# Kernel tuning notes

Hardware: AMD Instinct MI355X
Metric: run time of the kernel (lower is better)

## Reference

```python
import jax, jax.numpy as jnp
import numpy as np

N = 131072  # nodes
E = 4096    # edges (unused by forward)
MID = 32    # multiplicity of irreps_mid = 32x0e + 32x1o
NF = 128    # multiplicity of node_feat_irreps = 128x0e + 128x1o
INV_SQRT3 = 0.5773502691896258          # |w3j(1,1,0)| = |w3j(0,1,1)| = 1/sqrt(3)
PW_QQ_S = (1.0 / 2048.0) ** 0.5         # path weight: alpha = dim(0e)/ (32*32 + 32*32)
PW_QQ_V = (3.0 / 2048.0) ** 0.5         # path weight: alpha = dim(1o)/ (32*32 + 32*32)
PW_DOWN = (1.0 / 8192.0) ** 0.5         # path weight: alpha = dim(0e)/ (32*128 + 32*128)


def setup_inputs() -> dict:
    key = jax.random.key(0)
    ks = jax.random.split(key, 20)
    inp = {
        "node_feats": jax.random.normal(ks[0], (N, NF + 3 * NF), jnp.float32),
        "charges_0": jax.random.normal(ks[1], (N, 4), jnp.float32),
        "charges_induced": jax.random.normal(ks[2], (N, 4), jnp.float32),
        "edge_feats": jax.random.normal(ks[3], (E, 8), jnp.float32),
        "edge_attrs": jax.random.normal(ks[4], (E, 9), jnp.float32),
        "field_feats": jax.random.normal(ks[5], (N, 4), jnp.float32),
        "edge_index": jax.random.randint(ks[6], (2, E), 0, N, dtype=jnp.int32),
        "batch": jnp.sort(jax.random.randint(ks[7], (N,), 0, 64, dtype=jnp.int32)),
        # o3.Linear(1x0e+1x1o -> 32x0e+32x1o) params (fan_in = 1 per path -> norm 1)
        "Wa_s": jax.random.normal(ks[8], (1, MID), jnp.float32),
        "Wa_v": jax.random.normal(ks[9], (1, MID), jnp.float32),
        "b_a": jnp.zeros((MID,), jnp.float32),
        "Wb_s": jax.random.normal(ks[10], (1, MID), jnp.float32),
        "Wb_v": jax.random.normal(ks[11], (1, MID), jnp.float32),
        "b_b": jnp.zeros((MID,), jnp.float32),
        # FullyConnectedTensorProduct(mid, mid -> mid) uvw weights, one per CG path
        "W_ss": jax.random.normal(ks[12], (MID, MID, MID), jnp.float32),  # 0e x 0e -> 0e
        "W_vv": jax.random.normal(ks[13], (MID, MID, MID), jnp.float32),  # 1o x 1o -> 0e
        "W_sv": jax.random.normal(ks[14], (MID, MID, MID), jnp.float32),  # 0e x 1o -> 1o
        "W_vs": jax.random.normal(ks[15], (MID, MID, MID), jnp.float32),  # 1o x 0e -> 1o
        # FullyConnectedTensorProduct(mid, node_feats -> 1x0e) uvw weights
        "Wd_s": jax.random.normal(ks[16], (MID, NF), jnp.float32),        # 0e x 0e -> 0e
        "Wd_v": jax.random.normal(ks[17], (MID, NF), jnp.float32),        # 1o x 1o -> 0e
    }
    return inp


def reference(node_feats, charges_0, charges_induced, edge_feats, edge_attrs,
              field_feats, edge_index, batch,
              Wa_s, Wa_v, b_a, Wb_s, Wb_v, b_b,
              W_ss, W_vv, W_sv, W_vs, Wd_s, Wd_v):
    # split irreps blocks
    s0, v0 = charges_0[:, :1], charges_0[:, 1:4]            # [N,1], [N,3]
    si, vi = charges_induced[:, :1], charges_induced[:, 1:4]
    nf_s = node_feats[:, :NF]                               # [N,128]
    nf_v = node_feats[:, NF:].reshape(-1, NF, 3)            # [N,128,3]

    # charges = linear_qa(charges_induced) + linear_qb(charges_0)  (bias only on 0e)
    s = si @ Wa_s + b_a + s0 @ Wb_s + b_b                   # [N,32]
    v = (jnp.einsum('nui,uw->nwi', vi[:, None, :], Wa_v)
         + jnp.einsum('nui,uw->nwi', v0[:, None, :], Wb_v))  # [N,32,3]

    # qq = FullyConnectedTensorProduct(charges, charges) -> 32x0e + 32x1o
    qs = PW_QQ_S * (jnp.einsum('nu,nv,uvw->nw', s, s, W_ss)
                    + INV_SQRT3 * jnp.einsum('nui,nvi,uvw->nw', v, v, W_vv))      # [N,32]
    qv = (PW_QQ_V * INV_SQRT3) * (jnp.einsum('nu,nvi,uvw->nwi', s, v, W_sv)
                                  + jnp.einsum('nui,nv,uvw->nwi', v, s, W_vs))    # [N,32,3]

    # energy = FullyConnectedTensorProduct(qq, node_feats) -> 1x0e, then squeeze
    energy = PW_DOWN * (jnp.einsum('nu,nv,uv->n', qs, nf_s, Wd_s)
                        + INV_SQRT3 * jnp.einsum('nui,nvi,uv->n', qv, nf_v, Wd_v))  # [N]
    return energy
```

## Files before the change

kernel.cpp:

```cpp
#include <hip/hip_runtime.h>


#define TBLK 128
#define NNODES 131072

__global__ void precompute_coeff(
    const float* __restrict__ Wa_s, const float* __restrict__ Wa_v,
    const float* __restrict__ b_a,  const float* __restrict__ Wb_s,
    const float* __restrict__ Wb_v, const float* __restrict__ b_b,
    const float* __restrict__ W_ss, const float* __restrict__ W_vv,
    const float* __restrict__ W_sv, const float* __restrict__ W_vs,
    float* __restrict__ coeff)
{
  __shared__ float As[32], Bs[32], Cc[32], Av[32], Bv[32];
  const int t = threadIdx.x;
  if (t < 32) {
    As[t] = Wa_s[t]; Bs[t] = Wb_s[t]; Cc[t] = b_a[t] + b_b[t];
    Av[t] = Wa_v[t]; Bv[t] = Wb_v[t];
  }
  __syncthreads();
  const int w = t & 31;
  const int chunk = blockIdx.x * 8 + (t >> 5);
  float acc[15];
  #pragma unroll
  for (int k = 0; k < 15; ++k) acc[k] = 0.f;
  #pragma unroll
  for (int j = 0; j < 4; ++j) {
    const int p = chunk * 4 + j;
    const int u = p >> 5, v = p & 31;
    const float wss = W_ss[p * 32 + w];
    const float wvv = W_vv[p * 32 + w];
    const float wsv = W_sv[p * 32 + w];
    const float wvs = W_vs[p * 32 + w];
    const float au = As[u], bu = Bs[u], cu = Cc[u], pu = Av[u], qu = Bv[u];
    const float av = As[v], bv = Bs[v], cv = Cc[v], pv = Av[v], qv = Bv[v];
    acc[0]  = fmaf(au * av, wss, acc[0]);
    acc[1]  = fmaf(au * bv + bu * av, wss, acc[1]);
    acc[2]  = fmaf(bu * bv, wss, acc[2]);
    acc[3]  = fmaf(au * cv + cu * av, wss, acc[3]);
    acc[4]  = fmaf(bu * cv + cu * bv, wss, acc[4]);
    acc[5]  = fmaf(cu * cv, wss, acc[5]);
    acc[6]  = fmaf(pu * pv, wvv, acc[6]);
    acc[7]  = fmaf(pu * qv + qu * pv, wvv, acc[7]);
    acc[8]  = fmaf(qu * qv, wvv, acc[8]);
    acc[9]  = fmaf(au * pv, wsv, fmaf(pu * av, wvs, acc[9]));
    acc[10] = fmaf(au * qv, wsv, fmaf(qu * av, wvs, acc[10]));
    acc[11] = fmaf(bu * pv, wsv, fmaf(pu * bv, wvs, acc[11]));
    acc[12] = fmaf(bu * qv, wsv, fmaf(qu * bv, wvs, acc[12]));
    acc[13] = fmaf(cu * pv, wsv, fmaf(pu * cv, wvs, acc[13]));
    acc[14] = fmaf(cu * qv, wsv, fmaf(qu * cv, wvs, acc[14]));
  }
  #pragma unroll
  for (int k = 0; k < 15; ++k) atomicAdd(&coeff[k * 32 + w], acc[k]);
}

__global__ void precompute_M(
    const float* __restrict__ Wd_s, const float* __restrict__ Wd_v,
    const float* __restrict__ coeff,
    float* __restrict__ Ms, float* __restrict__ Mv)
{
  const int f = threadIdx.x;
  float as[9], av[6];
  #pragma unroll
  for (int k = 0; k < 9; ++k) as[k] = 0.f;
  #pragma unroll
  for (int k = 0; k < 6; ++k) av[k] = 0.f;
  for (int w = 0; w < 32; ++w) {
    const float wds = Wd_s[w * 128 + f];
    const float wdv = Wd_v[w * 128 + f];
    #pragma unroll
    for (int k = 0; k < 9; ++k) as[k] = fmaf(coeff[k * 32 + w], wds, as[k]);
    #pragma unroll
    for (int k = 0; k < 6; ++k) av[k] = fmaf(coeff[(9 + k) * 32 + w], wdv, av[k]);
  }
  const float sP = 1.0f / 4096.0f;
  const float sQ = 0.57735026918962576451f / 4096.0f;
  #pragma unroll
  for (int k = 0; k < 6; ++k) Ms[f * 16 + k] = as[k] * sP;
  #pragma unroll
  for (int k = 0; k < 3; ++k) Ms[f * 16 + 6 + k] = as[6 + k] * sQ;
  #pragma unroll
  for (int k = 0; k < 6; ++k) Mv[f * 8 + k] = av[k] * sQ;
}

__device__ __forceinline__ float wcomb9(const float* __restrict__ p,
    float m0, float m1, float m2, float a, float b,
    float m6, float m7, float m8)
{
  float r = p[5];
  r = fmaf(m0, p[0], r);
  r = fmaf(m1, p[1], r);
  r = fmaf(m2, p[2], r);
  r = fmaf(a,  p[3], r);
  r = fmaf(b,  p[4], r);
  r = fmaf(m6, p[6], r);
  r = fmaf(m7, p[7], r);
  r = fmaf(m8, p[8], r);
  return r;
}

template<int PHASE>
__device__ __forceinline__ void vtile_compute(
    const float4* __restrict__ tile4, const int t, const int swz, const int qb,
    const float* __restrict__ Mv,
    const float alpha, const float beta,
    const float g0, const float g1, const float g2,
    const float d0, const float d1, const float d2,
    float& e0, float& e1, float& e2, float& e3)
{
  #pragma unroll
  for (int j4 = 0; j4 < 16; ++j4) {
    const float4 x = tile4[t * 16 + (j4 ^ swz)];
    const float xs[4] = {x.x, x.y, x.z, x.w};
    #pragma unroll
    for (int e = 0; e < 4; ++e) {
      const int l = 4 * j4 + e;
      const int i = (PHASE + l) % 3;
      const int f = qb + (PHASE + l) / 3;
      const float* cv = Mv + f * 8;
      const float Wg = fmaf(alpha, cv[0], fmaf(beta, cv[2], cv[4]));
      const float Wd = fmaf(alpha, cv[1], fmaf(beta, cv[3], cv[5]));
      const float gs = (i == 0) ? g0 : ((i == 1) ? g1 : g2);
      const float ds = (i == 0) ? d0 : ((i == 1) ? d1 : d2);
      const float wv = fmaf(gs, Wg, ds * Wd);
      if      (e == 0) e0 = fmaf(xs[0], wv, e0);
      else if (e == 1) e1 = fmaf(xs[1], wv, e1);
      else if (e == 2) e2 = fmaf(xs[2], wv, e2);
      else             e3 = fmaf(xs[3], wv, e3);
    }
  }
}

__global__ __launch_bounds__(TBLK, 2) void energy_main(
    const float* __restrict__ nf,
    const float* __restrict__ ch0,
    const float* __restrict__ chi,
    const float* __restrict__ Ms,
    const float* __restrict__ Mv,
    float* __restrict__ out)
{
  __shared__ float4 tile4[TBLK * 16];
  const int t = threadIdx.x;
  const int node0 = blockIdx.x * TBLK;

  const float4 cc0 = reinterpret_cast<const float4*>(ch0)[node0 + t];
  const float4 cci = reinterpret_cast<const float4*>(chi)[node0 + t];
  const float alpha = cci.x, g0 = cci.y, g1 = cci.z, g2 = cci.w;
  const float beta  = cc0.x, d0 = cc0.y, d1 = cc0.z, d2 = cc0.w;
  const float m0 = alpha * alpha, m1 = alpha * beta, m2 = beta * beta;
  const float m6 = fmaf(g0, g0, fmaf(g1, g1, g2 * g2));
  const float m7 = fmaf(g0, d0, fmaf(g1, d1, g2 * d2));
  const float m8 = fmaf(d0, d0, fmaf(d1, d1, d2 * d2));

  const int lr = t >> 4;
  const int lc = t & 15;
  const int swz = t & 15;

  float e0 = 0.f, e1 = 0.f, e2 = 0.f, e3 = 0.f;

  for (int tl = 0; tl < 8; ++tl) {
    __syncthreads();
    const float* gsrc = nf + (size_t)node0 * 512 + tl * 64;
    #pragma unroll
    for (int p = 0; p < 16; ++p) {
      const int row = p * 8 + lr;
      const float4 v = reinterpret_cast<const float4*>(gsrc + (size_t)row * 512)[lc];
      tile4[row * 16 + (lc ^ (row & 15))] = v;
    }
    __syncthreads();

    if (tl < 2) {
      const int fbase = tl * 64;
      #pragma unroll
      for (int j4 = 0; j4 < 16; ++j4) {
        const float4 x = tile4[t * 16 + (j4 ^ swz)];
        const float* cp = Ms + (fbase + 4 * j4) * 16;
        e0 = fmaf(x.x, wcomb9(cp,      m0, m1, m2, alpha, beta, m6, m7, m8), e0);
        e1 = fmaf(x.y, wcomb9(cp + 16, m0, m1, m2, alpha, beta, m6, m7, m8), e1);
        e2 = fmaf(x.z, wcomb9(cp + 32, m0, m1, m2, alpha, beta, m6, m7, m8), e2);
        e3 = fmaf(x.w, wcomb9(cp + 48, m0, m1, m2, alpha, beta, m6, m7, m8), e3);
      }
    } else {
      const int k = tl - 2;
      const int qb = (k * 64) / 3;
      switch (k % 3) {
        case 0: vtile_compute<0>(tile4, t, swz, qb, Mv, alpha, beta, g0, g1, g2, d0, d1, d2, e0, e1, e2, e3); break;
        case 1: vtile_compute<1>(tile4, t, swz, qb, Mv, alpha, beta, g0, g1, g2, d0, d1, d2, e0, e1, e2, e3); break;
        default: vtile_compute<2>(tile4, t, swz, qb, Mv, alpha, beta, g0, g1, g2, d0, d1, d2, e0, e1, e2, e3); break;
      }
    }
  }
  out[node0 + t] = (e0 + e1) + (e2 + e3);
}

extern "C" void kernel_launch(void* const* d_in, const int* in_sizes, int n_in,
                              void* d_out, int out_size, void* d_ws, size_t ws_size,
                              hipStream_t stream)
{
  const float* node_feats      = (const float*)d_in[0];
  const float* charges_0       = (const float*)d_in[1];
  const float* charges_induced = (const float*)d_in[2];
  const float* Wa_s = (const float*)d_in[8];
  const float* Wa_v = (const float*)d_in[9];
  const float* b_a  = (const float*)d_in[10];
  const float* Wb_s = (const float*)d_in[11];
  const float* Wb_v = (const float*)d_in[12];
  const float* b_b  = (const float*)d_in[13];
  const float* W_ss = (const float*)d_in[14];
  const float* W_vv = (const float*)d_in[15];
  const float* W_sv = (const float*)d_in[16];
  const float* W_vs = (const float*)d_in[17];
  const float* Wd_s = (const float*)d_in[18];
  const float* Wd_v = (const float*)d_in[19];

  float* ws    = (float*)d_ws;
  float* Ms    = ws;
  float* Mv    = ws + 2048;
  float* coeff = ws + 3072;

  hipMemsetAsync(coeff, 0, 480 * sizeof(float), stream);
  precompute_coeff<<<32, 256, 0, stream>>>(Wa_s, Wa_v, b_a, Wb_s, Wb_v, b_b,
                                           W_ss, W_vv, W_sv, W_vs, coeff);
  precompute_M<<<1, 128, 0, stream>>>(Wd_s, Wd_v, coeff, Ms, Mv);
  energy_main<<<NNODES / TBLK, TBLK, 0, stream>>>(node_feats, charges_0,
                                                  charges_induced, Ms, Mv,
                                                  (float*)d_out);
}
```

Measured before the change: 447.7 us.

## Double-buffer node feature tiles via direct global-to-LDS loads and refactor vector math

The main kernel now stages 32-column tiles straight from global memory into LDS with the global_load_lds builtin, double-buffering so the next tile loads while the current one is computed. This replaces the old register-staged copy that had two barriers per tile. The vector path now accumulates the per-feature dot products P and Q and applies the alpha/beta weight combination once at the end, cutting FMAs per element. The atomic/memset coefficient reduction is replaced by a deterministic two-stage reduction through shared memory and a partial buffer. Risks include the full waitcnt(0) before each barrier serialising the pipeline and correctness of the swizzled LDS layout.

```diff
diff --git a/kernel.cpp b/kernel.cpp
--- a/kernel.cpp
+++ b/kernel.cpp
@@ -3,6 +3,12 @@
 
 #define TBLK 128
 #define NNODES 131072
+
+typedef __attribute__((address_space(1))) const void gas_void;
+typedef __attribute__((address_space(3))) void las_void;
+__device__ __forceinline__ void gl_lds16(const void* g, void* l) {
+  __builtin_amdgcn_global_load_lds((gas_void*)g, (las_void*)l, 16, 0, 0);
+}
 
 __global__ void precompute_coeff(
     const float* __restrict__ Wa_s, const float* __restrict__ Wa_v,
@@ -10,17 +16,19 @@
     const float* __restrict__ Wb_v, const float* __restrict__ b_b,
     const float* __restrict__ W_ss, const float* __restrict__ W_vv,
     const float* __restrict__ W_sv, const float* __restrict__ W_vs,
-    float* __restrict__ coeff)
-{
-  __shared__ float As[32], Bs[32], Cc[32], Av[32], Bv[32];
+    float* __restrict__ partial)
+{
+  __shared__ float As[32], Bs[32], Cc[32], Avv[32], Bvv[32];
+  __shared__ float red[8][480];
   const int t = threadIdx.x;
   if (t < 32) {
     As[t] = Wa_s[t]; Bs[t] = Wb_s[t]; Cc[t] = b_a[t] + b_b[t];
-    Av[t] = Wa_v[t]; Bv[t] = Wb_v[t];
+    Avv[t] = Wa_v[t]; Bvv[t] = Wb_v[t];
   }
   __syncthreads();
   const int w = t & 31;
-  const int chunk = blockIdx.x * 8 + (t >> 5);
+  const int grp = t >> 5;
+  const int chunk = blockIdx.x * 8 + grp;
   float acc[15];
   #pragma unroll
   for (int k = 0; k < 15; ++k) acc[k] = 0.f;
@@ -32,8 +40,8 @@
     const float wvv = W_vv[p * 32 + w];
     const float wsv = W_sv[p * 32 + w];
     const float wvs = W_vs[p * 32 + w];
-    const float au = As[u], bu = Bs[u], cu = Cc[u], pu = Av[u], qu = Bv[u];
-    const float av = As[v], bv = Bs[v], cv = Cc[v], pv = Av[v], qv = Bv[v];
+    const float au = As[u], bu = Bs[u], cu = Cc[u], pu = Avv[u], qu = Bvv[u];
+    const float av = As[v], bv = Bs[v], cv = Cc[v], pv = Avv[v], qv = Bvv[v];
     acc[0]  = fmaf(au * av, wss, acc[0]);
     acc[1]  = fmaf(au * bv + bu * av, wss, acc[1]);
     acc[2]  = fmaf(bu * bv, wss, acc[2]);
@@ -51,36 +59,53 @@
     acc[14] = fmaf(cu * qv, wsv, fmaf(qu * cv, wvs, acc[14]));
   }
   #pragma unroll
-  for (int k = 0; k < 15; ++k) atomicAdd(&coeff[k * 32 + w], acc[k]);
+  for (int k = 0; k < 15; ++k) red[grp][k * 32 + w] = acc[k];
+  __syncthreads();
+  for (int kk = grp; kk < 15; kk += 8) {
+    float s = 0.f;
+    #pragma unroll
+    for (int b = 0; b < 8; ++b) s += red[b][kk * 32 + w];
+    partial[blockIdx.x * 480 + kk * 32 + w] = s;
+  }
 }
 
 __global__ void precompute_M(
     const float* __restrict__ Wd_s, const float* __restrict__ Wd_v,
-    const float* __restrict__ coeff,
+    const float* __restrict__ partial,
     float* __restrict__ Ms, float* __restrict__ Mv)
 {
-  const int f = threadIdx.x;
-  float as[9], av[6];
-  #pragma unroll
-  for (int k = 0; k < 9; ++k) as[k] = 0.f;
-  #pragma unroll
-  for (int k = 0; k < 6; ++k) av[k] = 0.f;
-  for (int w = 0; w < 32; ++w) {
-    const float wds = Wd_s[w * 128 + f];
-    const float wdv = Wd_v[w * 128 + f];
-    #pragma unroll
-    for (int k = 0; k < 9; ++k) as[k] = fmaf(coeff[k * 32 + w], wds, as[k]);
-    #pragma unroll
-    for (int k = 0; k < 6; ++k) av[k] = fmaf(coeff[(9 + k) * 32 + w], wdv, av[k]);
-  }
-  const float sP = 1.0f / 4096.0f;
-  const float sQ = 0.57735026918962576451f / 4096.0f;
-  #pragma unroll
-  for (int k = 0; k < 6; ++k) Ms[f * 16 + k] = as[k] * sP;
-  #pragma unroll
-  for (int k = 0; k < 3; ++k) Ms[f * 16 + 6 + k] = as[6 + k] * sQ;
-  #pragma unroll
-  for (int k = 0; k < 6; ++k) Mv[f * 8 + k] = av[k] * sQ;
+  __shared__ float cf[480];
+  const int t = threadIdx.x;
+  if (t < 480) {
+    float s = 0.f;
+    for (int b = 0; b < 32; ++b) s += partial[b * 480 + t];
+    cf[t] = s;
+  }
+  __syncthreads();
+  if (t < 128) {
+    const int f = t;
+    float as[9], av[6];
+    #pragma unroll
+    for (int k = 0; k < 9; ++k) as[k] = 0.f;
+    #pragma unroll
+    for (int k = 0; k < 6; ++k) av[k] = 0.f;
+    for (int w = 0; w < 32; ++w) {
+      const float wds = Wd_s[w * 128 + f];
+      const float wdv = Wd_v[w * 128 + f];
+      #pragma unroll
+      for (int k = 0; k < 9; ++k) as[k] = fmaf(cf[k * 32 + w], wds, as[k]);
+      #pragma unroll
+      for (int k = 0; k < 6; ++k) av[k] = fmaf(cf[(9 + k) * 32 + w], wdv, av[k]);
+    }
+    const float sP = 1.0f / 4096.0f;
+    const float sQ = 0.57735026918962576451f / 4096.0f;
+    #pragma unroll
+    for (int k = 0; k < 6; ++k) Ms[f * 16 + k] = as[k] * sP;
+    #pragma unroll
+    for (int k = 0; k < 3; ++k) Ms[f * 16 + 6 + k] = as[6 + k] * sQ;
+    #pragma unroll
+    for (int k = 0; k < 6; ++k) Mv[f * 8 + k] = av[k] * sQ;
+  }
 }
 
 __device__ __forceinline__ float wcomb9(const float* __restrict__ p,
@@ -99,34 +124,57 @@
   return r;
 }
 
+__device__ __forceinline__ void stage_tile(
+    const float* __restrict__ nf, float4* __restrict__ buf,
+    int node0, int tl, int t)
+{
+  const int wv   = t >> 6;
+  const int lane = t & 63;
+  const int r_in = lane >> 3;
+  const int s_in = lane & 7;
+  #pragma unroll
+  for (int q = 0; q < 8; ++q) {
+    const int p   = wv * 8 + q;
+    const int row = p * 8 + r_in;
+    const int gs  = s_in ^ (r_in & 7);
+    const float4* g = reinterpret_cast<const float4*>(nf)
+                    + ((size_t)(node0 + row) * 128 + tl * 8 + gs);
+    gl_lds16(g, buf + p * 64);
+  }
+}
+
 template<int PHASE>
-__device__ __forceinline__ void vtile_compute(
-    const float4* __restrict__ tile4, const int t, const int swz, const int qb,
+__device__ __forceinline__ void vtile(
+    const float4* __restrict__ cur, int t, int fb,
     const float* __restrict__ Mv,
-    const float alpha, const float beta,
-    const float g0, const float g1, const float g2,
-    const float d0, const float d1, const float d2,
-    float& e0, float& e1, float& e2, float& e3)
-{
-  #pragma unroll
-  for (int j4 = 0; j4 < 16; ++j4) {
-    const float4 x = tile4[t * 16 + (j4 ^ swz)];
+    float g0, float g1, float g2, float d0, float d1, float d2,
+    float& P, float& Q,
+    float& SP0, float& SP2, float& SP4,
+    float& SQ1, float& SQ3, float& SQ5)
+{
+  const int sw = t & 7;
+  #pragma unroll
+  for (int j = 0; j < 8; ++j) {
+    const float4 x = cur[t * 8 + (j ^ sw)];
     const float xs[4] = {x.x, x.y, x.z, x.w};
     #pragma unroll
     for (int e = 0; e < 4; ++e) {
-      const int l = 4 * j4 + e;
+      const int l = 4 * j + e;
       const int i = (PHASE + l) % 3;
-      const int f = qb + (PHASE + l) / 3;
-      const float* cv = Mv + f * 8;
-      const float Wg = fmaf(alpha, cv[0], fmaf(beta, cv[2], cv[4]));
-      const float Wd = fmaf(alpha, cv[1], fmaf(beta, cv[3], cv[5]));
-      const float gs = (i == 0) ? g0 : ((i == 1) ? g1 : g2);
-      const float ds = (i == 0) ? d0 : ((i == 1) ? d1 : d2);
-      const float wv = fmaf(gs, Wg, ds * Wd);
-      if      (e == 0) e0 = fmaf(xs[0], wv, e0);
-      else if (e == 1) e1 = fmaf(xs[1], wv, e1);
-      else if (e == 2) e2 = fmaf(xs[2], wv, e2);
-      else             e3 = fmaf(xs[3], wv, e3);
+      const float gg = (i == 0) ? g0 : ((i == 1) ? g1 : g2);
+      const float dd = (i == 0) ? d0 : ((i == 1) ? d1 : d2);
+      P = fmaf(gg, xs[e], P);
+      Q = fmaf(dd, xs[e], Q);
+      if (i == 2) {
+        const float* cv = Mv + (fb + (PHASE + l) / 3) * 8;
+        SP0 = fmaf(cv[0], P, SP0);
+        SQ1 = fmaf(cv[1], Q, SQ1);
+        SP2 = fmaf(cv[2], P, SP2);
+        SQ3 = fmaf(cv[3], Q, SQ3);
+        SP4 = fmaf(cv[4], P, SP4);
+        SQ5 = fmaf(cv[5], Q, SQ5);
+        P = 0.f; Q = 0.f;
+      }
     }
   }
 }
@@ -139,12 +187,15 @@
     const float* __restrict__ Mv,
     float* __restrict__ out)
 {
-  __shared__ float4 tile4[TBLK * 16];
+  __shared__ float4 buf[2][1024];
   const int t = threadIdx.x;
   const int node0 = blockIdx.x * TBLK;
 
   const float4 cc0 = reinterpret_cast<const float4*>(ch0)[node0 + t];
   const float4 cci = reinterpret_cast<const float4*>(chi)[node0 + t];
+
+  stage_tile(nf, &buf[0][0], node0, 0, t);
+
   const float alpha = cci.x, g0 = cci.y, g1 = cci.z, g2 = cci.w;
   const float beta  = cc0.x, d0 = cc0.y, d1 = cc0.z, d2 = cc0.w;
   const float m0 = alpha * alpha, m1 = alpha * beta, m2 = beta * beta;
@@ -152,45 +203,43 @@
   const float m7 = fmaf(g0, d0, fmaf(g1, d1, g2 * d2));
   const float m8 = fmaf(d0, d0, fmaf(d1, d1, d2 * d2));
 
-  const int lr = t >> 4;
-  const int lc = t & 15;
-  const int swz = t & 15;
-
-  float e0 = 0.f, e1 = 0.f, e2 = 0.f, e3 = 0.f;
-
-  for (int tl = 0; tl < 8; ++tl) {
+  const int sw = t & 7;
+  float es0 = 0.f, es1 = 0.f, es2 = 0.f, es3 = 0.f;
+  float P = 0.f, Q = 0.f;
+  float SP0 = 0.f, SP2 = 0.f, SP4 = 0.f, SQ1 = 0.f, SQ3 = 0.f, SQ5 = 0.f;
+
+  #pragma unroll
+  for (int tl = 0; tl < 16; ++tl) {
+    __builtin_amdgcn_s_waitcnt(0);
     __syncthreads();
-    const float* gsrc = nf + (size_t)node0 * 512 + tl * 64;
-    #pragma unroll
-    for (int p = 0; p < 16; ++p) {
-      const int row = p * 8 + lr;
-      const float4 v = reinterpret_cast<const float4*>(gsrc + (size_t)row * 512)[lc];
-      tile4[row * 16 + (lc ^ (row & 15))] = v;
-    }
-    __syncthreads();
-
-    if (tl < 2) {
-      const int fbase = tl * 64;
+    if (tl < 15) stage_tile(nf, &buf[(tl + 1) & 1][0], node0, tl + 1, t);
+    const float4* cur = &buf[tl & 1][0];
+
+    if (tl < 4) {
+      const float* cp0 = Ms + tl * 32 * 16;
       #pragma unroll
-      for (int j4 = 0; j4 < 16; ++j4) {
-        const float4 x = tile4[t * 16 + (j4 ^ swz)];
-        const float* cp = Ms + (fbase + 4 * j4) * 16;
-        e0 = fmaf(x.x, wcomb9(cp,      m0, m1, m2, alpha, beta, m6, m7, m8), e0);
-        e1 = fmaf(x.y, wcomb9(cp + 16, m0, m1, m2, alpha, beta, m6, m7, m8), e1);
-        e2 = fmaf(x.z, wcomb9(cp + 32, m0, m1, m2, alpha, beta, m6, m7, m8), e2);
-        e3 = fmaf(x.w, wcomb9(cp + 48, m0, m1, m2, alpha, beta, m6, m7, m8), e3);
+      for (int j = 0; j < 8; ++j) {
+        const float4 x = cur[t * 8 + (j ^ sw)];
+        const float* cp = cp0 + j * 64;
+        es0 = fmaf(x.x, wcomb9(cp,      m0, m1, m2, alpha, beta, m6, m7, m8), es0);
+        es1 = fmaf(x.y, wcomb9(cp + 16, m0, m1, m2, alpha, beta, m6, m7, m8), es1);
+        es2 = fmaf(x.z, wcomb9(cp + 32, m0, m1, m2, alpha, beta, m6, m7, m8), es2);
+        es3 = fmaf(x.w, wcomb9(cp + 48, m0, m1, m2, alpha, beta, m6, m7, m8), es3);
       }
     } else {
-      const int k = tl - 2;
-      const int qb = (k * 64) / 3;
-      switch (k % 3) {
-        case 0: vtile_compute<0>(tile4, t, swz, qb, Mv, alpha, beta, g0, g1, g2, d0, d1, d2, e0, e1, e2, e3); break;
-        case 1: vtile_compute<1>(tile4, t, swz, qb, Mv, alpha, beta, g0, g1, g2, d0, d1, d2, e0, e1, e2, e3); break;
-        default: vtile_compute<2>(tile4, t, swz, qb, Mv, alpha, beta, g0, g1, g2, d0, d1, d2, e0, e1, e2, e3); break;
+      const int k  = tl - 4;
+      const int cb = 32 * k;
+      const int fb = cb / 3;
+      switch (cb % 3) {
+        case 0:  vtile<0>(cur, t, fb, Mv, g0, g1, g2, d0, d1, d2, P, Q, SP0, SP2, SP4, SQ1, SQ3, SQ5); break;
+        case 1:  vtile<1>(cur, t, fb, Mv, g0, g1, g2, d0, d1, d2, P, Q, SP0, SP2, SP4, SQ1, SQ3, SQ5); break;
+        default: vtile<2>(cur, t, fb, Mv, g0, g1, g2, d0, d1, d2, P, Q, SP0, SP2, SP4, SQ1, SQ3, SQ5); break;
       }
     }
   }
-  out[node0 + t] = (e0 + e1) + (e2 + e3);
+
+  const float ev = fmaf(alpha, SP0 + SQ1, fmaf(beta, SP2 + SQ3, SP4 + SQ5));
+  out[node0 + t] = (es0 + es1) + (es2 + es3) + ev;
 }
 
 extern "C" void kernel_launch(void* const* d_in, const int* in_sizes, int n_in,
@@ -213,15 +262,14 @@
   const float* Wd_s = (const float*)d_in[18];
   const float* Wd_v = (const float*)d_in[19];
 
-  float* ws    = (float*)d_ws;
-  float* Ms    = ws;
-  float* Mv    = ws + 2048;
-  float* coeff = ws + 3072;
-
-  hipMemsetAsync(coeff, 0, 480 * sizeof(float), stream);
+  float* ws      = (float*)d_ws;
+  float* Ms      = ws;
+  float* Mv      = ws + 2048;
+  float* partial = ws + 3072;
+
   precompute_coeff<<<32, 256, 0, stream>>>(Wa_s, Wa_v, b_a, Wb_s, Wb_v, b_b,
-                                           W_ss, W_vv, W_sv, W_vs, coeff);
-  precompute_M<<<1, 128, 0, stream>>>(Wd_s, Wd_v, coeff, Ms, Mv);
+                                           W_ss, W_vv, W_sv, W_vs, partial);
+  precompute_M<<<1, 512, 0, stream>>>(Wd_s, Wd_v, partial, Ms, Mv);
   energy_main<<<NNODES / TBLK, TBLK, 0, stream>>>(node_feats, charges_0,
                                                   charges_induced, Ms, Mv,
                                                   (float*)d_out);
```

New measurement: 434.5 us. 2.9% less time.
